# Kernel optimization log

Hardware: AMD Instinct MI355X
Metric: run time of the kernel (lower is better)

Reference implementation:

```python
import jax, jax.numpy as jnp
import numpy as np

B, C, D = 512, 1000, 512
K = 10


def setup_inputs() -> dict:
    key = jax.random.key(0)
    k1, k2, k3, k4, k5 = jax.random.split(key, 5)
    x = jax.random.normal(k1, (B, D), dtype=jnp.float32)
    protos = jax.random.normal(k2, (C, D), dtype=jnp.float32)
    # ex2/ex1 chosen so N*ex2^2 - ex1^2 > 0 (valid sqrt)
    ex2 = jax.random.uniform(k3, (C, D), dtype=jnp.float32) + 1.0
    ex1 = jax.random.uniform(k4, (C, D), dtype=jnp.float32) * 0.1
    cls_num = jax.random.randint(k5, (C,), 1, 100, dtype=jnp.int32)
    proto_label = jnp.arange(C, dtype=jnp.int32)
    return {"x": x, "protos": protos, "ex2": ex2, "ex1": ex1,
            "cls_num": cls_num, "proto_label": proto_label, "k_nearest": K}


def reference(x, protos, ex2, ex1, cls_num, proto_label, k_nearest):
    # rd: per-class, per-feature variance proxy  [C, D]
    N = cls_num[:, None].astype(ex2.dtype)
    rd = jnp.sqrt(N * ex2 ** 2 - ex1 ** 2)
    # softmax over feature dim of (rowmax - rd)
    rd = jax.nn.softmax(jnp.max(rd, axis=1, keepdims=True) - rd, axis=1)
    # weighted squared distances: [B, C, D] -> reduce D -> [B, C]
    diff = x[:, None, :] - protos[None, :, :]
    x_dists = diff ** 2 * rd[None, :, :]
    simi_mat = x_dists.sum(axis=2)  # [B, C]
    # k smallest distances (torch.topk largest=False)
    neg_vals, topk_index = jax.lax.top_k(-simi_mat, k_nearest)
    topk_vals = -neg_vals  # [B, K]
    topk_conf = topk_vals.sum(axis=1, keepdims=True) / topk_vals  # [B, K]
    # pick prototype with max confidence, map through label table
    temp = jnp.argmax(topk_conf, axis=1)  # [B]
    ans_index = jnp.take_along_axis(topk_index, temp[:, None], axis=1)[:, 0]
    predict = proto_label[ans_index]  # [B]
    return predict, topk_conf
```

## Files before the change

kernel.cpp:

```cpp
#include <hip/hip_runtime.h>
#include <math.h>
#include <float.h>

#define B_SZ 512
#define C_SZ 1000
#define D_SZ 512
#define K_TOP 10
#define K2 1024

#define SIMI_OFF 0

#define BM 128
#define BN 16
#define BK 32
#define LDA 40
#define LDB 1032

using f16x8 = __attribute__((ext_vector_type(8))) _Float16;
using f32x4 = __attribute__((ext_vector_type(4))) float;

#if __has_builtin(__builtin_amdgcn_exp2f)
#define FAST_EXP2(x) __builtin_amdgcn_exp2f(x)
#else
#define FAST_EXP2(x) exp2f(x)
#endif
#if __has_builtin(__builtin_amdgcn_sqrtf)
#define FAST_SQRT(x) __builtin_amdgcn_sqrtf(x)
#else
#define FAST_SQRT(x) sqrtf(x)
#endif
#define LOG2E 1.44269504088896340736f

__device__ __forceinline__ void split2(float v, _Float16& h, _Float16& l) {
    h = (_Float16)v;
    l = (_Float16)(v - (float)h);
}

__global__ __launch_bounds__(512, 2) void fused_kernel(const float* __restrict__ x,
                                                       const float* __restrict__ protos,
                                                       const float* __restrict__ ex2,
                                                       const float* __restrict__ ex1,
                                                       const int* __restrict__ cls_num,
                                                       float* __restrict__ simi) {
    __shared__ __align__(16) _Float16 Ah[BM][LDA];
    __shared__ __align__(16) _Float16 Al[BM][LDA];
    __shared__ __align__(16) _Float16 BSh[BN][LDB];
    __shared__ __align__(16) _Float16 BSl[BN][LDB];
    __shared__ float t3s[BN];

    const int tid  = threadIdx.x;
    const int lane = tid & 63;
    const int w    = tid >> 6;
    const int cx = blockIdx.x & 63;
    const int by = blockIdx.x >> 6;
    const int c0 = cx * BN;
    const int b0 = by * BM;
    if (c0 >= C_SZ) return;

    #pragma unroll
    for (int r = 0; r < 2; r++) {
        const int lc = w * 2 + r;
        const int c  = c0 + lc;
        if (c < C_SZ) {
            const size_t rb = (size_t)c * D_SZ + lane * 8;
            float e2v[8], e1v[8], pv[8];
            *(float4*)&e2v[0] = *(const float4*)(ex2 + rb);
            *(float4*)&e2v[4] = *(const float4*)(ex2 + rb + 4);
            *(float4*)&e1v[0] = *(const float4*)(ex1 + rb);
            *(float4*)&e1v[4] = *(const float4*)(ex1 + rb + 4);
            *(float4*)&pv[0]  = *(const float4*)(protos + rb);
            *(float4*)&pv[4]  = *(const float4*)(protos + rb + 4);
            const float N = (float)cls_num[c];

            float v[8], mn = FLT_MAX;
            #pragma unroll
            for (int k = 0; k < 8; k++) {
                v[k] = FAST_SQRT(N * e2v[k] * e2v[k] - e1v[k] * e1v[k]);
                mn = fminf(mn, v[k]);
            }
            #pragma unroll
            for (int off = 1; off < 64; off <<= 1) mn = fminf(mn, __shfl_xor(mn, off));

            float ev[8], s = 0.f, te = 0.f;
            #pragma unroll
            for (int k = 0; k < 8; k++) {
                ev[k] = FAST_EXP2((mn - v[k]) * LOG2E);
                s += ev[k];
                te = fmaf(ev[k] * pv[k], pv[k], te);
            }
            #pragma unroll
            for (int off = 1; off < 64; off <<= 1) {
                s  += __shfl_xor(s, off);
                te += __shfl_xor(te, off);
            }
            const float inv = 1.0f / s;
            if (lane == 0) t3s[lc] = te * inv;

            f16x8 h1, l1, h2, l2;
            #pragma unroll
            for (int k = 0; k < 8; k++) {
                const float rdv = ev[k] * inv;
                const float w2  = -2.0f * rdv * pv[k];
                _Float16 hh, ll;
                split2(rdv, hh, ll); h1[k] = hh; l1[k] = ll;
                split2(w2,  hh, ll); h2[k] = hh; l2[k] = ll;
            }
            const int d = lane * 8;
            *(f16x8*)&BSh[lc][d]         = h1;
            *(f16x8*)&BSh[lc][D_SZ + d]  = h2;
            *(f16x8*)&BSl[lc][d]         = l1;
            *(f16x8*)&BSl[lc][D_SZ + d]  = l2;
        } else {
            f16x8 z;
            #pragma unroll
            for (int k = 0; k < 8; k++) z[k] = (_Float16)0.f;
            const int d = lane * 8;
            *(f16x8*)&BSh[lc][d]        = z;
            *(f16x8*)&BSh[lc][D_SZ + d] = z;
            *(f16x8*)&BSl[lc][d]        = z;
            *(f16x8*)&BSl[lc][D_SZ + d] = z;
        }
    }
    __syncthreads();

    const int srow = tid >> 2;
    const int sseg = (tid & 3) * 8;
    const int mw = w * 16;
    const int lr = lane & 15;
    const int kg = lane >> 4;

    f32x4 acc;
    #pragma unroll
    for (int r = 0; r < 4; r++) acc[r] = 0.f;

    for (int ch = 0; ch < K2 / BK; ch++) {
        const bool sq = (ch < 16);
        const int kx = (sq ? ch * BK : ch * BK - D_SZ) + sseg;

        float4 a0 = *(const float4*)(x + (size_t)(b0 + srow) * D_SZ + kx);
        float4 a1 = *(const float4*)(x + (size_t)(b0 + srow) * D_SZ + kx + 4);
        if (sq) {
            a0.x *= a0.x; a0.y *= a0.y; a0.z *= a0.z; a0.w *= a0.w;
            a1.x *= a1.x; a1.y *= a1.y; a1.z *= a1.z; a1.w *= a1.w;
        }
        const float av[8] = {a0.x, a0.y, a0.z, a0.w, a1.x, a1.y, a1.z, a1.w};
        f16x8 ah, al;
        #pragma unroll
        for (int j = 0; j < 8; j++) {
            _Float16 hh, ll;
            split2(av[j], hh, ll);
            ah[j] = hh; al[j] = ll;
        }

        __syncthreads();
        *(f16x8*)&Ah[srow][sseg] = ah;
        *(f16x8*)&Al[srow][sseg] = al;
        __syncthreads();

        const f16x8 fah = *(const f16x8*)&Ah[mw + lr][kg * 8];
        const f16x8 fal = *(const f16x8*)&Al[mw + lr][kg * 8];
        const f16x8 fbh = *(const f16x8*)&BSh[lr][ch * BK + kg * 8];
        const f16x8 fbl = *(const f16x8*)&BSl[lr][ch * BK + kg * 8];

        acc = __builtin_amdgcn_mfma_f32_16x16x32_f16(fal, fbl, acc, 0, 0, 0);
        acc = __builtin_amdgcn_mfma_f32_16x16x32_f16(fah, fbl, acc, 0, 0, 0);
        acc = __builtin_amdgcn_mfma_f32_16x16x32_f16(fal, fbh, acc, 0, 0, 0);
        acc = __builtin_amdgcn_mfma_f32_16x16x32_f16(fah, fbh, acc, 0, 0, 0);
    }

    const int c = c0 + lr;
    if (c < C_SZ) {
        const float t3v = t3s[lr];
        #pragma unroll
        for (int r = 0; r < 4; r++) {
            const int b = b0 + mw + kg * 4 + r;
            simi[(size_t)b * C_SZ + c] = acc[r] + t3v;
        }
    }
}

__global__ __launch_bounds__(256) void topk_kernel(const float* __restrict__ ws,
                                                   const int* __restrict__ proto_label,
                                                   float* __restrict__ out) {
    const float* simi = ws + SIMI_OFF;
    const int wid = threadIdx.x >> 6;
    const int lane = threadIdx.x & 63;
    const int b = blockIdx.x * 4 + wid;

    float vals[16];
    #pragma unroll
    for (int j = 0; j < 16; j++) {
        const int c = lane + j * 64;
        vals[j] = (c < C_SZ) ? simi[(size_t)b * C_SZ + c] : FLT_MAX;
    }

    float kv[K_TOP];
    int ki[K_TOP];
    for (int t = 0; t < K_TOP; t++) {
        float bv = FLT_MAX;
        int bi = 0x7fffffff;
        #pragma unroll
        for (int j = 0; j < 16; j++) {
            const int c = lane + j * 64;
            if (vals[j] < bv) { bv = vals[j]; bi = c; }
        }
        #pragma unroll
        for (int off = 1; off < 64; off <<= 1) {
            const float ov = __shfl_xor(bv, off);
            const int oi = __shfl_xor(bi, off);
            if (ov < bv || (ov == bv && oi < bi)) { bv = ov; bi = oi; }
        }
        kv[t] = bv;
        ki[t] = bi;
        if ((bi & 63) == lane) vals[bi >> 6] = FLT_MAX;
    }

    if (lane == 0) {
        float S = 0.f;
        #pragma unroll
        for (int t = 0; t < K_TOP; t++) S += kv[t];
        float conf[K_TOP];
        #pragma unroll
        for (int t = 0; t < K_TOP; t++) {
            conf[t] = S / kv[t];
            out[B_SZ + b * K_TOP + t] = conf[t];
        }
        int best = 0;
        for (int t = 1; t < K_TOP; t++)
            if (conf[t] > conf[best]) best = t;
        out[b] = (float)proto_label[ki[best]];
    }
}

extern "C" void kernel_launch(void* const* d_in, const int* in_sizes, int n_in,
                              void* d_out, int out_size, void* d_ws, size_t ws_size,
                              hipStream_t stream) {
    const float* x           = (const float*)d_in[0];
    const float* protos      = (const float*)d_in[1];
    const float* ex2         = (const float*)d_in[2];
    const float* ex1         = (const float*)d_in[3];
    const int*   cls_num     = (const int*)d_in[4];
    const int*   proto_label = (const int*)d_in[5];

    float* ws  = (float*)d_ws;
    float* out = (float*)d_out;

    fused_kernel<<<256, 512, 0, stream>>>(x, protos, ex2, ex1, cls_num,
                                          ws + SIMI_OFF);

    topk_kernel<<<B_SZ / 4, 256, 0, stream>>>(ws, proto_label, out);
}
```

Measured before the change: 104.4 us.

## Double the K chunk and prefetch next x chunk into registers

Raises the K step from 32 to 64, so each loop iteration does two MFMA sub-steps and the number of barrier pairs is halved. The next x chunk is loaded from global memory into registers before the current chunk is processed, hiding load latency behind the split/MFMA work. The first chunk load is also issued before the prototype-weight preprocessing. Launch bounds drop to one block per SM hint, which allows more registers per thread at the cost of potentially lower occupancy.

```diff
diff --git a/kernel.cpp b/kernel.cpp
--- a/kernel.cpp
+++ b/kernel.cpp
@@ -12,8 +12,8 @@
 
 #define BM 128
 #define BN 16
-#define BK 32
-#define LDA 40
+#define BK 64
+#define LDA 72
 #define LDB 1032
 
 using f16x8 = __attribute__((ext_vector_type(8))) _Float16;
@@ -36,7 +36,7 @@
     l = (_Float16)(v - (float)h);
 }
 
-__global__ __launch_bounds__(512, 2) void fused_kernel(const float* __restrict__ x,
+__global__ __launch_bounds__(512, 1) void fused_kernel(const float* __restrict__ x,
                                                        const float* __restrict__ protos,
                                                        const float* __restrict__ ex2,
                                                        const float* __restrict__ ex1,
@@ -56,6 +56,21 @@
     const int c0 = cx * BN;
     const int b0 = by * BM;
     if (c0 >= C_SZ) return;
+
+    const int srow = tid >> 2;
+    const int scol = (tid & 3) * 16;
+
+    auto load_chunk = [&](int ch, float4* dst) {
+        const int kx = (ch < 8 ? ch * BK : ch * BK - D_SZ) + scol;
+        const float* xp = x + (size_t)(b0 + srow) * D_SZ + kx;
+        dst[0] = *(const float4*)(xp);
+        dst[1] = *(const float4*)(xp + 4);
+        dst[2] = *(const float4*)(xp + 8);
+        dst[3] = *(const float4*)(xp + 12);
+    };
+
+    float4 cur[4], nxt[4];
+    load_chunk(0, cur);
 
     #pragma unroll
     for (int r = 0; r < 2; r++) {
@@ -123,8 +138,6 @@
     }
     __syncthreads();
 
-    const int srow = tid >> 2;
-    const int sseg = (tid & 3) * 8;
     const int mw = w * 16;
     const int lr = lane & 15;
     const int kg = lane >> 4;
@@ -134,38 +147,50 @@
     for (int r = 0; r < 4; r++) acc[r] = 0.f;
 
     for (int ch = 0; ch < K2 / BK; ch++) {
-        const bool sq = (ch < 16);
-        const int kx = (sq ? ch * BK : ch * BK - D_SZ) + sseg;
-
-        float4 a0 = *(const float4*)(x + (size_t)(b0 + srow) * D_SZ + kx);
-        float4 a1 = *(const float4*)(x + (size_t)(b0 + srow) * D_SZ + kx + 4);
+        if (ch + 1 < K2 / BK) load_chunk(ch + 1, nxt);
+
+        const bool sq = (ch < 8);
+        float av[16];
+        *(float4*)&av[0]  = cur[0];
+        *(float4*)&av[4]  = cur[1];
+        *(float4*)&av[8]  = cur[2];
+        *(float4*)&av[12] = cur[3];
         if (sq) {
-            a0.x *= a0.x; a0.y *= a0.y; a0.z *= a0.z; a0.w *= a0.w;
-            a1.x *= a1.x; a1.y *= a1.y; a1.z *= a1.z; a1.w *= a1.w;
-        }
-        const float av[8] = {a0.x, a0.y, a0.z, a0.w, a1.x, a1.y, a1.z, a1.w};
-        f16x8 ah, al;
-        #pragma unroll
-        for (int j = 0; j < 8; j++) {
+            #pragma unroll
+            for (int k = 0; k < 16; k++) av[k] *= av[k];
+        }
+        f16x8 ah0, ah1, al0, al1;
+        #pragma unroll
+        for (int k = 0; k < 8; k++) {
             _Float16 hh, ll;
-            split2(av[j], hh, ll);
-            ah[j] = hh; al[j] = ll;
+            split2(av[k], hh, ll);     ah0[k] = hh; al0[k] = ll;
+            split2(av[k + 8], hh, ll); ah1[k] = hh; al1[k] = ll;
         }
 
         __syncthreads();
-        *(f16x8*)&Ah[srow][sseg] = ah;
-        *(f16x8*)&Al[srow][sseg] = al;
+        *(f16x8*)&Ah[srow][scol]     = ah0;
+        *(f16x8*)&Ah[srow][scol + 8] = ah1;
+        *(f16x8*)&Al[srow][scol]     = al0;
+        *(f16x8*)&Al[srow][scol + 8] = al1;
         __syncthreads();
 
-        const f16x8 fah = *(const f16x8*)&Ah[mw + lr][kg * 8];
-        const f16x8 fal = *(const f16x8*)&Al[mw + lr][kg * 8];
-        const f16x8 fbh = *(const f16x8*)&BSh[lr][ch * BK + kg * 8];
-        const f16x8 fbl = *(const f16x8*)&BSl[lr][ch * BK + kg * 8];
-
-        acc = __builtin_amdgcn_mfma_f32_16x16x32_f16(fal, fbl, acc, 0, 0, 0);
-        acc = __builtin_amdgcn_mfma_f32_16x16x32_f16(fah, fbl, acc, 0, 0, 0);
-        acc = __builtin_amdgcn_mfma_f32_16x16x32_f16(fal, fbh, acc, 0, 0, 0);
-        acc = __builtin_amdgcn_mfma_f32_16x16x32_f16(fah, fbh, acc, 0, 0, 0);
+        #pragma unroll
+        for (int sub = 0; sub < 2; sub++) {
+            const int kc = sub * 32 + kg * 8;
+            const f16x8 fah = *(const f16x8*)&Ah[mw + lr][kc];
+            const f16x8 fal = *(const f16x8*)&Al[mw + lr][kc];
+            const f16x8 fbh = *(const f16x8*)&BSh[lr][ch * BK + kc];
+            const f16x8 fbl = *(const f16x8*)&BSl[lr][ch * BK + kc];
+            acc = __builtin_amdgcn_mfma_f32_16x16x32_f16(fal, fbl, acc, 0, 0, 0);
+            acc = __builtin_amdgcn_mfma_f32_16x16x32_f16(fah, fbl, acc, 0, 0, 0);
+            acc = __builtin_amdgcn_mfma_f32_16x16x32_f16(fal, fbh, acc, 0, 0, 0);
+            acc = __builtin_amdgcn_mfma_f32_16x16x32_f16(fah, fbh, acc, 0, 0, 0);
+        }
+
+        if (ch + 1 < K2 / BK) {
+            cur[0] = nxt[0]; cur[1] = nxt[1];
+            cur[2] = nxt[2]; cur[3] = nxt[3];
+        }
     }
 
     const int c = c0 + lr;
```

After: 96.59 us. 1.08x faster.
